# Kernel optimization log

Hardware: AMD Instinct MI355X
Metric: run time of the kernel (lower is better)

Reference implementation:

```python
import jax, jax.numpy as jnp
import numpy as np

N_NODES = 100000
N_EDGES = 800000
IN_FEATS = 128
N_HIDDEN = 128
N_CLASSES = 64


def setup_inputs() -> dict:
    key = jax.random.key(0)
    k = jax.random.split(key, 6)
    x = jax.random.normal(k[0], (N_NODES, IN_FEATS), dtype=jnp.float32)
    src = jax.random.randint(k[1], (N_EDGES,), 0, N_NODES, dtype=jnp.int32)
    dst = jax.random.randint(k[2], (N_EDGES,), 0, N_NODES, dtype=jnp.int32)
    W_neigh = jax.random.normal(k[3], (IN_FEATS, N_HIDDEN), dtype=jnp.float32) * (1.0 / np.sqrt(IN_FEATS))
    b_neigh = jnp.zeros((N_HIDDEN,), dtype=jnp.float32)
    W_out = jax.random.normal(k[4], (N_HIDDEN, N_CLASSES), dtype=jnp.float32) * (1.0 / np.sqrt(N_HIDDEN))
    b_out = jnp.zeros((N_CLASSES,), dtype=jnp.float32)
    return {"x": x, "src": src, "dst": dst, "W_neigh": W_neigh, "b_neigh": b_neigh,
            "W_out": W_out, "b_out": b_out}


def reference(x, src, dst, W_neigh, b_neigh, W_out, b_out):
    # DGL SAGEConv with 'gcn' aggregator:
    #   h_neigh[v] = (sum_{u->v} x[u] + x[v]) / (in_deg(v) + 1)
    #   h = h_neigh @ W_neigh + b_neigh
    deg = jax.ops.segment_sum(jnp.ones_like(dst, dtype=x.dtype), dst, num_segments=N_NODES)
    agg = jax.ops.segment_sum(x[src], dst, num_segments=N_NODES)  # [N, F] irregular gather+scatter
    h_neigh = (agg + x) / (deg + 1.0)[:, None]
    h = h_neigh @ W_neigh + b_neigh
    emb = jax.nn.relu(h)
    # dropout is identity in eval/reference mode
    out = emb @ W_out + b_out
    return (out, emb)
```

## Files before the change

kernel.cpp:

```cpp
#include <hip/hip_runtime.h>
#include <hip/hip_bf16.h>

#define N_NODES 100000
#define N_EDGES 800000
#define F 128
#define C_OUT 64
#define CAP 48
#define DUMMY N_NODES

typedef __bf16 bf16x8 __attribute__((ext_vector_type(8)));
typedef __bf16 bf16x4 __attribute__((ext_vector_type(4)));
typedef __bf16 bf16x2 __attribute__((ext_vector_type(2)));
typedef float f32x4 __attribute__((ext_vector_type(4)));

__global__ __launch_bounds__(256) void prep(const float* __restrict__ x,
                                            const int* __restrict__ src,
                                            const int* __restrict__ dst,
                                            float* __restrict__ emb,
                                            int* __restrict__ cnt,
                                            const float* __restrict__ Wn,
                                            const float* __restrict__ Wo,
                                            __bf16* __restrict__ Wn_s,
                                            __bf16* __restrict__ Wo_s,
                                            __bf16* __restrict__ xb,
                                            int zero_dummy) {
    const int t = blockIdx.x * 256 + threadIdx.x;

#pragma unroll
    for (int k = 0; k < 4; k++) {
        const int i = k * 800000 + t;
        const float4 v = ((const float4*)x)[i];
        bf16x4 b;
        b.x = (__bf16)v.x; b.y = (__bf16)v.y; b.z = (__bf16)v.z; b.w = (__bf16)v.w;
        *(bf16x4*)(xb + (size_t)i * 4) = b;
    }

    if (zero_dummy && t < 32) {
        int2 z = make_int2(0, 0);
        ((int2*)(xb + (size_t)N_NODES * F))[t] = z;
    }

    const int d = dst[t];
    const int slot = atomicAdd(cnt + d, 1);
    if (slot < CAP) ((int*)(emb + (size_t)d * F))[slot] = src[t];

    if (t < 3072) {
        const float* W;
        __bf16* Ws;
        int g, ncols;
        if (t < 2048) { W = Wn; Ws = Wn_s; g = t;        ncols = 128; }
        else          { W = Wo; Ws = Wo_s; g = t - 2048; ncols = 64;  }
        const int l = g & 63;
        const int kb = (g >> 6) & 3;
        const int nb = g >> 8;
        const int q = l >> 4, m = l & 15;
        const int n = nb * 16 + m;
        __bf16 v[8];
#pragma unroll
        for (int j = 0; j < 8; j++) {
            const int k = kb * 32 + q * 8 + j;
            v[j] = (__bf16)W[(size_t)k * ncols + n];
        }
        *(bf16x8*)(Ws + (size_t)g * 8) = *(bf16x8*)v;
    }
}

#define ACC4(bk, j, acc)                                                      \
    {                                                                         \
        const int4 s4 = *(const int4*)((bk) + (j));                           \
        const bf16x2 v0 = *(const bf16x2*)(xb + (size_t)s4.x * F + 2 * lane); \
        const bf16x2 v1 = *(const bf16x2*)(xb + (size_t)s4.y * F + 2 * lane); \
        const bf16x2 v2 = *(const bf16x2*)(xb + (size_t)s4.z * F + 2 * lane); \
        const bf16x2 v3 = *(const bf16x2*)(xb + (size_t)s4.w * F + 2 * lane); \
        acc.x += (float)v0.x + (float)v1.x + (float)v2.x + (float)v3.x;       \
        acc.y += (float)v0.y + (float)v1.y + (float)v2.y + (float)v3.y;       \
    }

#define ACC1(bk, j, acc)                                                       \
    {                                                                          \
        const int s = (bk)[j];                                                 \
        const bf16x2 v = *(const bf16x2*)(xb + (size_t)s * F + 2 * lane);      \
        acc.x += (float)v.x;                                                   \
        acc.y += (float)v.y;                                                   \
    }

__global__ __launch_bounds__(256, 6) void sage_fused(const __bf16* __restrict__ xb,
                                                     const int* __restrict__ cnt,
                                                     const __bf16* __restrict__ Wn_s,
                                                     const __bf16* __restrict__ Wo_s,
                                                     const float* __restrict__ bn,
                                                     const float* __restrict__ bo,
                                                     float* __restrict__ out,
                                                     float* emb) {
    __shared__ __align__(16) __bf16 Hs[4][16][136];
    const int w = threadIdx.x >> 6;
    const int lane = threadIdx.x & 63;
    const int node0 = (blockIdx.x * 4 + w) * 16;
    if (node0 >= N_NODES) return;
    const int q = lane >> 4, m = lane & 15;
    __bf16(*H)[136] = Hs[w];

    for (int i = 0; i < 16; i += 4) {
        const int na = node0 + i;
        const int4 dg = *(const int4*)(cnt + na);
        const int n0 = dg.x < CAP ? dg.x : CAP, n1 = dg.y < CAP ? dg.y : CAP;
        const int n2 = dg.z < CAP ? dg.z : CAP, n3 = dg.w < CAP ? dg.w : CAP;
        const int p0 = (n0 + 3) & ~3, p1 = (n1 + 3) & ~3;
        const int p2 = (n2 + 3) & ~3, p3 = (n3 + 3) & ~3;
        const int* bk0 = (const int*)(emb + (size_t)(na + 0) * F);
        const int* bk1 = (const int*)(emb + (size_t)(na + 1) * F);
        const int* bk2 = (const int*)(emb + (size_t)(na + 2) * F);
        const int* bk3 = (const int*)(emb + (size_t)(na + 3) * F);
        const bf16x2 s0 = *(const bf16x2*)(xb + (size_t)(na + 0) * F + 2 * lane);
        const bf16x2 s1 = *(const bf16x2*)(xb + (size_t)(na + 1) * F + 2 * lane);
        const bf16x2 s2 = *(const bf16x2*)(xb + (size_t)(na + 2) * F + 2 * lane);
        const bf16x2 s3 = *(const bf16x2*)(xb + (size_t)(na + 3) * F + 2 * lane);
        if (lane < 4) {
            const int nn = lane == 0 ? n0 : lane == 1 ? n1 : lane == 2 ? n2 : n3;
            const int pp = lane == 0 ? p0 : lane == 1 ? p1 : lane == 2 ? p2 : p3;
            int* bw = (int*)(lane == 0 ? bk0 : lane == 1 ? bk1 : lane == 2 ? bk2 : bk3);
            for (int s = nn; s < pp; s++) bw[s] = DUMMY;
        }
        asm volatile("s_waitcnt vmcnt(0)" ::: "memory");

        float2 a0 = make_float2((float)s0.x, (float)s0.y);
        float2 a1 = make_float2((float)s1.x, (float)s1.y);
        float2 a2 = make_float2((float)s2.x, (float)s2.y);
        float2 a3 = make_float2((float)s3.x, (float)s3.y);
        const int jmax = max(max(p0, p1), max(p2, p3));
        for (int j = 0; j < jmax; j += 4) {
            if (j < p0) ACC4(bk0, j, a0);
            if (j < p1) ACC4(bk1, j, a1);
            if (j < p2) ACC4(bk2, j, a2);
            if (j < p3) ACC4(bk3, j, a3);
        }
        const float i0 = 1.0f / (float)(dg.x + 1), i1 = 1.0f / (float)(dg.y + 1);
        const float i2 = 1.0f / (float)(dg.z + 1), i3 = 1.0f / (float)(dg.w + 1);
        bf16x2 h0, h1, h2, h3;
        h0.x = (__bf16)(a0.x * i0); h0.y = (__bf16)(a0.y * i0);
        h1.x = (__bf16)(a1.x * i1); h1.y = (__bf16)(a1.y * i1);
        h2.x = (__bf16)(a2.x * i2); h2.y = (__bf16)(a2.y * i2);
        h3.x = (__bf16)(a3.x * i3); h3.y = (__bf16)(a3.y * i3);
        *(bf16x2*)&H[i + 0][2 * lane] = h0;
        *(bf16x2*)&H[i + 1][2 * lane] = h1;
        *(bf16x2*)&H[i + 2][2 * lane] = h2;
        *(bf16x2*)&H[i + 3][2 * lane] = h3;
    }

    bf16x8 afr[4];
#pragma unroll
    for (int kb = 0; kb < 4; kb++)
        afr[kb] = *(const bf16x8*)&H[m][kb * 32 + q * 8];
    asm volatile("s_waitcnt lgkmcnt(0)" ::: "memory");

    float* Ef = (float*)&H[0][0];
    const int srow = lane >> 2;
    const int sc4 = (lane & 3) * 4;
    f32x4 o[4];
#pragma unroll
    for (int nb = 0; nb < 4; nb++) o[nb] = (f32x4){0.f, 0.f, 0.f, 0.f};

#pragma unroll
    for (int half = 0; half < 2; half++) {
#pragma unroll
        for (int nb2 = 0; nb2 < 4; nb2++) {
            const int nb = half * 4 + nb2;
            f32x4 c = {0.f, 0.f, 0.f, 0.f};
#pragma unroll
            for (int kb = 0; kb < 4; kb++) {
                const bf16x8 b = *(const bf16x8*)(Wn_s + ((size_t)(nb * 4 + kb) * 64 + lane) * 8);
                c = __builtin_amdgcn_mfma_f32_16x16x32_bf16(afr[kb], b, c, 0, 0, 0);
            }
            const float bias = bn[nb * 16 + m];
#pragma unroll
            for (int r = 0; r < 4; r++)
                Ef[(q * 4 + r) * 68 + nb2 * 16 + m] = fmaxf(c[r] + bias, 0.f);
        }
        asm volatile("s_waitcnt lgkmcnt(0)" ::: "memory");
#pragma unroll
        for (int it = 0; it < 4; it++) {
            const f32x4 v = *(const f32x4*)&Ef[srow * 68 + it * 16 + sc4];
            *(f32x4*)&emb[(size_t)(node0 + srow) * F + half * 64 + it * 16 + sc4] = v;
        }
#pragma unroll
        for (int t2 = 0; t2 < 2; t2++) {
            const int kb = half * 2 + t2;
            const f32x4 f0 = *(const f32x4*)&Ef[m * 68 + t2 * 32 + q * 8];
            const f32x4 f1 = *(const f32x4*)&Ef[m * 68 + t2 * 32 + q * 8 + 4];
            bf16x8 a2f;
            a2f[0] = (__bf16)f0[0]; a2f[1] = (__bf16)f0[1];
            a2f[2] = (__bf16)f0[2]; a2f[3] = (__bf16)f0[3];
            a2f[4] = (__bf16)f1[0]; a2f[5] = (__bf16)f1[1];
            a2f[6] = (__bf16)f1[2]; a2f[7] = (__bf16)f1[3];
#pragma unroll
            for (int nb = 0; nb < 4; nb++) {
                const bf16x8 b = *(const bf16x8*)(Wo_s + ((size_t)(nb * 4 + kb) * 64 + lane) * 8);
                o[nb] = __builtin_amdgcn_mfma_f32_16x16x32_bf16(a2f, b, o[nb], 0, 0, 0);
            }
        }
        asm volatile("s_waitcnt lgkmcnt(0)" ::: "memory");
    }

#pragma unroll
    for (int nb = 0; nb < 4; nb++) {
        const float bias = bo[nb * 16 + m];
#pragma unroll
        for (int r = 0; r < 4; r++)
            Ef[(q * 4 + r) * 68 + nb * 16 + m] = o[nb][r] + bias;
    }
    asm volatile("s_waitcnt lgkmcnt(0)" ::: "memory");
#pragma unroll
    for (int it = 0; it < 4; it++) {
        const f32x4 v = *(const f32x4*)&Ef[srow * 68 + it * 16 + sc4];
        *(f32x4*)&out[(size_t)(node0 + srow) * C_OUT + it * 16 + sc4] = v;
    }
}

__global__ __launch_bounds__(256, 8) void sage1_fb(const __bf16* __restrict__ xb,
                                                   const int* __restrict__ cnt,
                                                   const __bf16* __restrict__ Wn_s,
                                                   const float* __restrict__ bn,
                                                   float* emb) {
    __shared__ __align__(16) __bf16 Hs[4][16][136];
    const int w = threadIdx.x >> 6;
    const int lane = threadIdx.x & 63;
    const int node0 = (blockIdx.x * 4 + w) * 16;
    if (node0 >= N_NODES) return;
    const int q = lane >> 4, m = lane & 15;
    __bf16(*H)[136] = Hs[w];

    for (int i = 0; i < 16; i += 2) {
        const int nodeA = node0 + i, nodeB = nodeA + 1;
        const int degA = cnt[nodeA], degB = cnt[nodeB];
        const int nA = degA < CAP ? degA : CAP;
        const int nB = degB < CAP ? degB : CAP;
        const bf16x2 sA = *(const bf16x2*)(xb + (size_t)nodeA * F + 2 * lane);
        const bf16x2 sB = *(const bf16x2*)(xb + (size_t)nodeB * F + 2 * lane);
        float2 accA = make_float2((float)sA.x, (float)sA.y);
        float2 accB = make_float2((float)sB.x, (float)sB.y);
        const int* bkA = (const int*)(emb + (size_t)nodeA * F);
        const int* bkB = (const int*)(emb + (size_t)nodeB * F);
        int ja = 0, jb = 0;
        while ((ja + 4 <= nA) && (jb + 4 <= nB)) {
            ACC4(bkA, ja, accA);
            ACC4(bkB, jb, accB);
            ja += 4; jb += 4;
        }
        while (ja + 4 <= nA) { ACC4(bkA, ja, accA); ja += 4; }
        while (jb + 4 <= nB) { ACC4(bkB, jb, accB); jb += 4; }
        while ((ja < nA) && (jb < nB)) { ACC1(bkA, ja, accA); ACC1(bkB, jb, accB); ja++; jb++; }
        while (ja < nA) { ACC1(bkA, ja, accA); ja++; }
        while (jb < nB) { ACC1(bkB, jb, accB); jb++; }
        const float invA = 1.0f / (float)(degA + 1);
        const float invB = 1.0f / (float)(degB + 1);
        bf16x2 hA, hB;
        hA.x = (__bf16)(accA.x * invA); hA.y = (__bf16)(accA.y * invA);
        hB.x = (__bf16)(accB.x * invB); hB.y = (__bf16)(accB.y * invB);
        *(bf16x2*)&H[i][2 * lane] = hA;
        *(bf16x2*)&H[i + 1][2 * lane] = hB;
    }

    bf16x8 a[4];
#pragma unroll
    for (int kb = 0; kb < 4; kb++)
        a[kb] = *(const bf16x8*)&H[m][kb * 32 + q * 8];
    asm volatile("s_waitcnt lgkmcnt(0)" ::: "memory");

    float* Ef = (float*)&H[0][0];
    const int srow = lane >> 2;
    const int sc4 = (lane & 3) * 4;
#pragma unroll
    for (int half = 0; half < 2; half++) {
#pragma unroll
        for (int nb2 = 0; nb2 < 4; nb2++) {
            const int nb = half * 4 + nb2;
            f32x4 c = {0.f, 0.f, 0.f, 0.f};
#pragma unroll
            for (int kb = 0; kb < 4; kb++) {
                const bf16x8 b = *(const bf16x8*)(Wn_s + ((size_t)(nb * 4 + kb) * 64 + lane) * 8);
                c = __builtin_amdgcn_mfma_f32_16x16x32_bf16(a[kb], b, c, 0, 0, 0);
            }
            const float bias = bn[nb * 16 + m];
#pragma unroll
            for (int r = 0; r < 4; r++)
                Ef[(q * 4 + r) * 68 + nb2 * 16 + m] = fmaxf(c[r] + bias, 0.f);
        }
        asm volatile("s_waitcnt lgkmcnt(0)" ::: "memory");
#pragma unroll
        for (int it = 0; it < 4; it++) {
            const f32x4 v = *(const f32x4*)&Ef[srow * 68 + it * 16 + sc4];
            *(f32x4*)&emb[(size_t)(node0 + srow) * F + half * 64 + it * 16 + sc4] = v;
        }
        if (half == 0) asm volatile("s_waitcnt lgkmcnt(0)" ::: "memory");
    }
}

__global__ __launch_bounds__(256, 6) void sage2_fb(const float* __restrict__ emb,
                                                   const __bf16* __restrict__ Wo_s,
                                                   const float* __restrict__ bo,
                                                   float* __restrict__ out) {
    const int w = threadIdx.x >> 6;
    const int lane = threadIdx.x & 63;
    const int node0 = (blockIdx.x * 4 + w) * 16;
    if (node0 >= N_NODES) return;
    const int q = lane >> 4, m = lane & 15;

    bf16x8 a[4];
#pragma unroll
    for (int kb = 0; kb < 4; kb++) {
        const float* p = emb + (size_t)(node0 + m) * F + kb * 32 + q * 8;
        const float4 f0 = *(const float4*)(p);
        const float4 f1 = *(const float4*)(p + 4);
        bf16x8 v;
        v[0] = (__bf16)f0.x; v[1] = (__bf16)f0.y; v[2] = (__bf16)f0.z; v[3] = (__bf16)f0.w;
        v[4] = (__bf16)f1.x; v[5] = (__bf16)f1.y; v[6] = (__bf16)f1.z; v[7] = (__bf16)f1.w;
        a[kb] = v;
    }
#pragma unroll
    for (int nb = 0; nb < 4; nb++) {
        f32x4 c = {0.f, 0.f, 0.f, 0.f};
#pragma unroll
        for (int kb = 0; kb < 4; kb++) {
            const bf16x8 b = *(const bf16x8*)(Wo_s + ((size_t)(nb * 4 + kb) * 64 + lane) * 8);
            c = __builtin_amdgcn_mfma_f32_16x16x32_bf16(a[kb], b, c, 0, 0, 0);
        }
        const int col = nb * 16 + m;
        const float bias = bo[col];
#pragma unroll
        for (int r = 0; r < 4; r++) {
            const int node = node0 + q * 4 + r;
            out[(size_t)node * C_OUT + col] = c[r] + bias;
        }
    }
}

extern "C" void kernel_launch(void* const* d_in, const int* in_sizes, int n_in,
                              void* d_out, int out_size, void* d_ws, size_t ws_size,
                              hipStream_t stream) {
    const float* x  = (const float*)d_in[0];
    const int* src  = (const int*)d_in[1];
    const int* dst  = (const int*)d_in[2];
    const float* Wn = (const float*)d_in[3];
    const float* bn = (const float*)d_in[4];
    const float* Wo = (const float*)d_in[5];
    const float* bo = (const float*)d_in[6];

    float* out = (float*)d_out;
    float* emb = out + (size_t)N_NODES * C_OUT;

    int* cnt = (int*)d_ws;
    __bf16* Wn_s = (__bf16*)((char*)d_ws + 400000);
    __bf16* Wo_s = Wn_s + 128 * 128;
    __bf16* xb_ws = (__bf16*)((char*)d_ws + 449152);

    const size_t WS_NEEDED = 449152 + (size_t)(N_NODES + 1) * F * 2;
    const bool fused = ws_size >= WS_NEEDED;

    hipMemsetAsync(cnt, 0, N_NODES * sizeof(int), stream);

    if (fused) {
        prep<<<3125, 256, 0, stream>>>(x, src, dst, emb, cnt, Wn, Wo, Wn_s, Wo_s,
                                       xb_ws, 1);
        sage_fused<<<(N_NODES + 63) / 64, 256, 0, stream>>>(xb_ws, cnt, Wn_s, Wo_s,
                                                            bn, bo, out, emb);
    } else {
        __bf16* xb = (__bf16*)d_out;
        prep<<<3125, 256, 0, stream>>>(x, src, dst, emb, cnt, Wn, Wo, Wn_s, Wo_s,
                                       xb, 0);
        sage1_fb<<<(N_NODES + 63) / 64, 256, 0, stream>>>(xb, cnt, Wn_s, bn, emb);
        sage2_fb<<<(N_NODES + 63) / 64, 256, 0, stream>>>(emb, Wo_s, bo, out);
    }
}
```

Baseline: 214.8 us.

## Gather eight nodes at once with prefetched edge indices and masked dummy loads

The aggregation loop now processes 8 nodes per group instead of 4. It prefetches the next int4 of neighbour indices while gathering the current ones, and masks unused slots to the dummy row instead of writing padding into the bucket. This exposes more independent loads per wave to hide gather latency. In exchange every node runs up to the group maximum degree with dummy loads, and register pressure rises, so launch bounds drop from 6 to 4 waves per SIMD and occupancy falls.

```diff
diff --git a/kernel.cpp b/kernel.cpp
--- a/kernel.cpp
+++ b/kernel.cpp
@@ -84,7 +84,7 @@
         acc.y += (float)v.y;                                                   \
     }
 
-__global__ __launch_bounds__(256, 6) void sage_fused(const __bf16* __restrict__ xb,
+__global__ __launch_bounds__(256, 4) void sage_fused(const __bf16* __restrict__ xb,
                                                      const int* __restrict__ cnt,
                                                      const __bf16* __restrict__ Wn_s,
                                                      const __bf16* __restrict__ Wo_s,
@@ -100,51 +100,69 @@
     const int q = lane >> 4, m = lane & 15;
     __bf16(*H)[136] = Hs[w];
 
-    for (int i = 0; i < 16; i += 4) {
-        const int na = node0 + i;
-        const int4 dg = *(const int4*)(cnt + na);
-        const int n0 = dg.x < CAP ? dg.x : CAP, n1 = dg.y < CAP ? dg.y : CAP;
-        const int n2 = dg.z < CAP ? dg.z : CAP, n3 = dg.w < CAP ? dg.w : CAP;
-        const int p0 = (n0 + 3) & ~3, p1 = (n1 + 3) & ~3;
-        const int p2 = (n2 + 3) & ~3, p3 = (n3 + 3) & ~3;
-        const int* bk0 = (const int*)(emb + (size_t)(na + 0) * F);
-        const int* bk1 = (const int*)(emb + (size_t)(na + 1) * F);
-        const int* bk2 = (const int*)(emb + (size_t)(na + 2) * F);
-        const int* bk3 = (const int*)(emb + (size_t)(na + 3) * F);
-        const bf16x2 s0 = *(const bf16x2*)(xb + (size_t)(na + 0) * F + 2 * lane);
-        const bf16x2 s1 = *(const bf16x2*)(xb + (size_t)(na + 1) * F + 2 * lane);
-        const bf16x2 s2 = *(const bf16x2*)(xb + (size_t)(na + 2) * F + 2 * lane);
-        const bf16x2 s3 = *(const bf16x2*)(xb + (size_t)(na + 3) * F + 2 * lane);
-        if (lane < 4) {
-            const int nn = lane == 0 ? n0 : lane == 1 ? n1 : lane == 2 ? n2 : n3;
-            const int pp = lane == 0 ? p0 : lane == 1 ? p1 : lane == 2 ? p2 : p3;
-            int* bw = (int*)(lane == 0 ? bk0 : lane == 1 ? bk1 : lane == 2 ? bk2 : bk3);
-            for (int s = nn; s < pp; s++) bw[s] = DUMMY;
-        }
-        asm volatile("s_waitcnt vmcnt(0)" ::: "memory");
-
-        float2 a0 = make_float2((float)s0.x, (float)s0.y);
-        float2 a1 = make_float2((float)s1.x, (float)s1.y);
-        float2 a2 = make_float2((float)s2.x, (float)s2.y);
-        float2 a3 = make_float2((float)s3.x, (float)s3.y);
-        const int jmax = max(max(p0, p1), max(p2, p3));
-        for (int j = 0; j < jmax; j += 4) {
-            if (j < p0) ACC4(bk0, j, a0);
-            if (j < p1) ACC4(bk1, j, a1);
-            if (j < p2) ACC4(bk2, j, a2);
-            if (j < p3) ACC4(bk3, j, a3);
-        }
-        const float i0 = 1.0f / (float)(dg.x + 1), i1 = 1.0f / (float)(dg.y + 1);
-        const float i2 = 1.0f / (float)(dg.z + 1), i3 = 1.0f / (float)(dg.w + 1);
-        bf16x2 h0, h1, h2, h3;
-        h0.x = (__bf16)(a0.x * i0); h0.y = (__bf16)(a0.y * i0);
-        h1.x = (__bf16)(a1.x * i1); h1.y = (__bf16)(a1.y * i1);
-        h2.x = (__bf16)(a2.x * i2); h2.y = (__bf16)(a2.y * i2);
-        h3.x = (__bf16)(a3.x * i3); h3.y = (__bf16)(a3.y * i3);
-        *(bf16x2*)&H[i + 0][2 * lane] = h0;
-        *(bf16x2*)&H[i + 1][2 * lane] = h1;
-        *(bf16x2*)&H[i + 2][2 * lane] = h2;
-        *(bf16x2*)&H[i + 3][2 * lane] = h3;
+    for (int g = 0; g < 2; g++) {
+        const int base = node0 + g * 8;
+        const int4 dA = *(const int4*)(cnt + base);
+        const int4 dB = *(const int4*)(cnt + base + 4);
+        const int deg[8] = {dA.x, dA.y, dA.z, dA.w, dB.x, dB.y, dB.z, dB.w};
+        int n[8];
+        const int* bk[8];
+#pragma unroll
+        for (int t = 0; t < 8; t++) {
+            n[t] = deg[t] < CAP ? deg[t] : CAP;
+            bk[t] = (const int*)(emb + (size_t)(base + t) * F);
+        }
+        int4 qd[8];
+#pragma unroll
+        for (int t = 0; t < 8; t++) qd[t] = *(const int4*)bk[t];
+        bf16x2 sv[8];
+#pragma unroll
+        for (int t = 0; t < 8; t++)
+            sv[t] = *(const bf16x2*)(xb + (size_t)(base + t) * F + 2 * lane);
+        float2 a[8];
+#pragma unroll
+        for (int t = 0; t < 8; t++)
+            a[t] = make_float2((float)sv[t].x, (float)sv[t].y);
+        int nmax = 0;
+#pragma unroll
+        for (int t = 0; t < 8; t++) nmax = n[t] > nmax ? n[t] : nmax;
+
+        for (int j = 0; j < nmax; j += 4) {
+            const int jn = (j + 4) <= 44 ? (j + 4) : 44;
+            int4 r[8];
+#pragma unroll
+            for (int t = 0; t < 8; t++) r[t] = *(const int4*)(bk[t] + jn);
+            bf16x2 v[32];
+#pragma unroll
+            for (int t = 0; t < 8; t++) {
+                const int e0 = (j + 0 < n[t]) ? qd[t].x : DUMMY;
+                const int e1 = (j + 1 < n[t]) ? qd[t].y : DUMMY;
+                const int e2 = (j + 2 < n[t]) ? qd[t].z : DUMMY;
+                const int e3 = (j + 3 < n[t]) ? qd[t].w : DUMMY;
+                v[4 * t + 0] = *(const bf16x2*)(xb + (size_t)e0 * F + 2 * lane);
+                v[4 * t + 1] = *(const bf16x2*)(xb + (size_t)e1 * F + 2 * lane);
+                v[4 * t + 2] = *(const bf16x2*)(xb + (size_t)e2 * F + 2 * lane);
+                v[4 * t + 3] = *(const bf16x2*)(xb + (size_t)e3 * F + 2 * lane);
+            }
+#pragma unroll
+            for (int t = 0; t < 8; t++) {
+                a[t].x += (float)v[4 * t + 0].x + (float)v[4 * t + 1].x +
+                          (float)v[4 * t + 2].x + (float)v[4 * t + 3].x;
+                a[t].y += (float)v[4 * t + 0].y + (float)v[4 * t + 1].y +
+                          (float)v[4 * t + 2].y + (float)v[4 * t + 3].y;
+            }
+#pragma unroll
+            for (int t = 0; t < 8; t++) qd[t] = r[t];
+        }
+
+#pragma unroll
+        for (int t = 0; t < 8; t++) {
+            const float inv = 1.0f / (float)(deg[t] + 1);
+            bf16x2 h;
+            h.x = (__bf16)(a[t].x * inv);
+            h.y = (__bf16)(a[t].y * inv);
+            *(bf16x2*)&H[g * 8 + t][2 * lane] = h;
+        }
     }
 
     bf16x8 afr[4];
```

New measurement: 238.0 us. 1.11x slower.
